# Optimization experiments

Measured on AMD Instinct MI355X. Metric: run time of the kernel, lower is better.

The kernel has to match this reference:

```python
import jax, jax.numpy as jnp
import numpy as np
import math

NUM_HEADS = 16


def setup_inputs() -> dict:
    key = jax.random.key(0)
    ks = jax.random.split(key, 5)
    B, C, H = 2, 2048, 1024
    return {
        "x": jax.random.normal(ks[0], (B, C, H), dtype=jnp.float32),
        "Wqkv_w": jax.random.normal(ks[1], (3 * H, H), dtype=jnp.float32) * (1.0 / math.sqrt(H)),
        "Wqkv_b": jax.random.normal(ks[2], (3 * H,), dtype=jnp.float32) * 0.02,
        "Wo_w": jax.random.normal(ks[3], (H, H), dtype=jnp.float32) * (1.0 / math.sqrt(H)),
        "Wo_b": jax.random.normal(ks[4], (H,), dtype=jnp.float32) * 0.02,
    }


def reference(x, Wqkv_w, Wqkv_b, Wo_w, Wo_b):
    B, C, H = x.shape
    nh = NUM_HEADS
    hd = H // nh
    # QKV projection (torch Linear: x @ W.T + b)
    qkv = x @ Wqkv_w.T + Wqkv_b                      # [B, C, 3H]
    qkv = qkv.reshape(B, C, 3, nh, hd)
    qkv = jnp.transpose(qkv, (2, 0, 3, 1, 4))        # [3, B, nh, C, hd]
    q, k, v = qkv[0], qkv[1], qkv[2]
    scale = 1.0 / math.sqrt(hd)
    att = jnp.einsum('bhqd,bhkd->bhqk', q, k) * scale  # [B, nh, C, C]
    causal = jnp.triu(jnp.ones((C, C), dtype=bool), k=1)  # True above diagonal
    att = jnp.where(causal[None, None], jnp.float32(-jnp.inf), att)
    att = jax.nn.softmax(att, axis=-1)
    # dropout p set to 0 (eval-mode math)
    out = jnp.einsum('bhqk,bhkd->bhqd', att, v)       # [B, nh, C, hd]
    out = jnp.transpose(out, (0, 2, 1, 3)).reshape(B, C, H)
    return out @ Wo_w.T + Wo_b
```

## Files before the change

### kernel.cpp

```cpp
#include <hip/hip_runtime.h>
#include <hip/hip_bf16.h>
#include <math.h>

typedef unsigned short u16;
typedef __attribute__((ext_vector_type(8))) __bf16 bf16x8;
typedef __attribute__((ext_vector_type(4))) float f32x4;
typedef __attribute__((ext_vector_type(8))) unsigned short u16x8;
typedef __attribute__((ext_vector_type(4))) unsigned int u32x4;

__device__ __forceinline__ u16 f2bf(float f) {
  union { float f; unsigned u; } x; x.f = f;
  unsigned r = x.u + 0x7fffu + ((x.u >> 16) & 1u);
  return (u16)(r >> 16);
}

__device__ __forceinline__ void gload16(const u16* g, u16* l) {
  __builtin_amdgcn_global_load_lds(
      (const __attribute__((address_space(1))) void*)g,
      (__attribute__((address_space(3))) void*)l, 16, 0, 0);
}

#define MFMA16(a, b, c) __builtin_amdgcn_mfma_f32_16x16x32_bf16((a), (b), (c), 0, 0, 0)

#define QSCALE 0.18033688011112043f

__global__ __launch_bounds__(256) void cast_all_kernel(
    const float* __restrict__ x, const float* __restrict__ wqkv,
    const float* __restrict__ wo, u16* __restrict__ xb,
    u16* __restrict__ wqb, u16* __restrict__ wob) {
  int i = blockIdx.x * 256 + threadIdx.x;
  const float* src; u16* dst;
  if (i < 1048576)      { src = x;    dst = xb;  }
  else if (i < 1835008) { src = wqkv; dst = wqb; i -= 1048576; }
  else                  { src = wo;   dst = wob; i -= 1835008; }
  f32x4 v = *(const f32x4*)(src + (size_t)i * 4);
  u16 o0 = f2bf(v[0]), o1 = f2bf(v[1]), o2 = f2bf(v[2]), o3 = f2bf(v[3]);
  unsigned lo = (unsigned)o0 | ((unsigned)o1 << 16);
  unsigned hi = (unsigned)o2 | ((unsigned)o3 << 16);
  ((unsigned*)dst)[(size_t)i * 2] = lo;
  ((unsigned*)dst)[(size_t)i * 2 + 1] = hi;
}

__device__ __forceinline__ void gemm_bt_128(
    const u16* __restrict__ A, const u16* __restrict__ B, int K, int m0, int n0,
    u16* As, u16* Bs, f32x4 acc[4][4]) {
  const int tid = threadIdx.x;
  const int lane = tid & 63;
  const int wr = tid >> 7;
  const int wc = (tid >> 6) & 1;
  for (int k0 = 0; k0 < K; k0 += 64) {
    #pragma unroll
    for (int it = 0; it < 4; ++it) {
      int c = it * 256 + tid;
      int row = c >> 3;
      int ko = (c & 7) << 3;
      gload16(A + (size_t)(m0 + row) * K + (k0 + ko), As + c * 8);
      gload16(B + (size_t)(n0 + row) * K + (k0 + ko), Bs + c * 8);
    }
    __syncthreads();
    #pragma unroll
    for (int kk = 0; kk < 2; ++kk) {
      bf16x8 a[4], b[4];
      #pragma unroll
      for (int m = 0; m < 4; ++m)
        a[m] = *(const bf16x8*)(As + ((wr * 64 + m * 16 + (lane & 15)) * 64 +
                                      kk * 32 + ((lane >> 4) << 3)));
      #pragma unroll
      for (int n = 0; n < 4; ++n)
        b[n] = *(const bf16x8*)(Bs + ((wc * 64 + n * 16 + (lane & 15)) * 64 +
                                      kk * 32 + ((lane >> 4) << 3)));
      #pragma unroll
      for (int m = 0; m < 4; ++m)
        #pragma unroll
        for (int n = 0; n < 4; ++n)
          acc[m][n] = MFMA16(a[m], b[n], acc[m][n]);
    }
    __syncthreads();
  }
}

__global__ __launch_bounds__(256) void gemm_qkv_kernel(
    const u16* __restrict__ X, const u16* __restrict__ W, const float* __restrict__ bias,
    u16* __restrict__ Qb, u16* __restrict__ Kb, u16* __restrict__ Vb) {
  __shared__ __align__(16) u16 As[128 * 64];
  __shared__ __align__(16) u16 Bs[128 * 64];
  f32x4 acc[4][4];
  #pragma unroll
  for (int m = 0; m < 4; ++m)
    #pragma unroll
    for (int n = 0; n < 4; ++n) acc[m][n] = (f32x4){0.f, 0.f, 0.f, 0.f};
  const int m0 = blockIdx.y * 128;
  const int n0 = blockIdx.x * 128;
  gemm_bt_128(X, W, 1024, m0, n0, As, Bs, acc);
  const int lane = threadIdx.x & 63;
  const int wr = threadIdx.x >> 7, wc = (threadIdx.x >> 6) & 1;
  #pragma unroll
  for (int m = 0; m < 4; ++m) {
    #pragma unroll
    for (int n = 0; n < 4; ++n) {
      #pragma unroll
      for (int j = 0; j < 4; ++j) {
        int row = m0 + wr * 64 + m * 16 + ((lane >> 4) << 2) + j;
        int col = n0 + wc * 64 + n * 16 + (lane & 15);
        float v = acc[m][n][j] + bias[col];
        int which = col >> 10;
        int rem = col & 1023;
        int h = rem >> 6, d = rem & 63;
        int bb = row >> 11, q = row & 2047;
        if (which == 0) v *= QSCALE;
        u16* dst = (which == 0) ? Qb : (which == 1 ? Kb : Vb);
        dst[((size_t)((bb * 16 + h) * 2048 + q)) * 64 + d] = f2bf(v);
      }
    }
  }
}

__global__ __launch_bounds__(256) void gemm_out_kernel(
    const u16* __restrict__ Ain, const u16* __restrict__ W, const float* __restrict__ bias,
    float* __restrict__ out) {
  __shared__ __align__(16) u16 As[64 * 64];
  __shared__ __align__(16) u16 Bs[128 * 64];
  const int tid = threadIdx.x;
  const int lane = tid & 63;
  const int wc = tid >> 6;
  const int m0 = blockIdx.y * 64;
  const int n0 = blockIdx.x * 128;
  f32x4 acc[4][2] = {};
  for (int k0 = 0; k0 < 1024; k0 += 64) {
    #pragma unroll
    for (int it = 0; it < 2; ++it) {
      int c = it * 256 + tid;
      gload16(Ain + (size_t)(m0 + (c >> 3)) * 1024 + k0 + ((c & 7) << 3), As + c * 8);
    }
    #pragma unroll
    for (int it = 0; it < 4; ++it) {
      int c = it * 256 + tid;
      gload16(W + (size_t)(n0 + (c >> 3)) * 1024 + k0 + ((c & 7) << 3), Bs + c * 8);
    }
    __syncthreads();
    #pragma unroll
    for (int kk = 0; kk < 2; ++kk) {
      bf16x8 a[4], b[2];
      #pragma unroll
      for (int m = 0; m < 4; ++m)
        a[m] = *(const bf16x8*)(As + ((m * 16 + (lane & 15)) * 64 +
                                      kk * 32 + ((lane >> 4) << 3)));
      #pragma unroll
      for (int n = 0; n < 2; ++n)
        b[n] = *(const bf16x8*)(Bs + ((wc * 32 + n * 16 + (lane & 15)) * 64 +
                                      kk * 32 + ((lane >> 4) << 3)));
      #pragma unroll
      for (int m = 0; m < 4; ++m)
        #pragma unroll
        for (int n = 0; n < 2; ++n)
          acc[m][n] = MFMA16(a[m], b[n], acc[m][n]);
    }
    __syncthreads();
  }
  #pragma unroll
  for (int m = 0; m < 4; ++m)
    #pragma unroll
    for (int n = 0; n < 2; ++n)
      #pragma unroll
      for (int j = 0; j < 4; ++j) {
        int row = m0 + m * 16 + ((lane >> 4) << 2) + j;
        int col = n0 + wc * 32 + n * 16 + (lane & 15);
        out[(size_t)row * 1024 + col] = acc[m][n][j] + bias[col];
      }
}

__device__ __forceinline__ void attn_one(
    const u16* __restrict__ Qh, const u16* __restrict__ Kh, const u16* __restrict__ Vh,
    u16* __restrict__ Ob, int bb, int h, int qt,
    u16 (*Ks)[64 * 64], u16 (*Vt)[64 * 64]) {
  const int tid = threadIdx.x, lane = tid & 63, w = tid >> 6;
  const int g = lane >> 4, q15 = lane & 15;

  bf16x8 qf[2];
  const int qrow = qt * 64 + w * 16 + q15;
  #pragma unroll
  for (int kk = 0; kk < 2; ++kk)
    qf[kk] = *(const bf16x8*)(Qh + (size_t)qrow * 64 + kk * 32 + g * 8);

  f32x4 acc_o[4];
  #pragma unroll
  for (int n = 0; n < 4; ++n) acc_o[n] = (f32x4){0.f, 0.f, 0.f, 0.f};
  float m_run = -INFINITY, l_run = 0.f;

  const int nt = qt + 1;

  auto stageK = [&](int t, int buf) {
    #pragma unroll
    for (int it = 0; it < 2; ++it) {
      int c = it * 256 + tid;
      int row = c >> 3, b8 = c & 7;
      gload16(Kh + (size_t)(t * 64 + row) * 64 + ((b8 ^ (row & 7)) << 3),
              Ks[buf] + c * 8);
    }
  };

  stageK(0, 0);
  #pragma unroll
  for (int it = 0; it < 2; ++it) {
    int kloc = it * 32 + (tid >> 3);
    int d0 = (tid & 7) << 3;
    u16x8 v = *(const u16x8*)(Vh + (size_t)kloc * 64 + d0);
    #pragma unroll
    for (int i = 0; i < 8; ++i) {
      int d = d0 + i;
      int fv = (d + (d >> 3)) & 7;
      Vt[0][d * 64 + (((kloc >> 3) ^ fv) << 3) + (kloc & 7)] = v[i];
    }
  }
  __syncthreads();

  for (int t = 0; t < nt; ++t) {
    const int cur = t & 1;
    const bool pre = (t + 1 < nt);
    u16x8 vreg[2];
    if (pre) {
      stageK(t + 1, cur ^ 1);
      #pragma unroll
      for (int it = 0; it < 2; ++it) {
        int kloc = it * 32 + (tid >> 3);
        int d0 = (tid & 7) << 3;
        vreg[it] = *(const u16x8*)(Vh + (size_t)((t + 1) * 64 + kloc) * 64 + d0);
      }
    }

    f32x4 accs[4];
    __builtin_amdgcn_s_setprio(1);
    #pragma unroll
    for (int cb = 0; cb < 4; ++cb) {
      accs[cb] = (f32x4){0.f, 0.f, 0.f, 0.f};
      #pragma unroll
      for (int kk = 0; kk < 2; ++kk) {
        int row = cb * 16 + q15;
        int kblk = kk * 4 + g;
        bf16x8 kf = *(const bf16x8*)(Ks[cur] + row * 64 + ((kblk ^ (row & 7)) << 3));
        accs[cb] = MFMA16(kf, qf[kk], accs[cb]);
      }
    }
    __builtin_amdgcn_s_setprio(0);
    if (t == nt - 1) {
      #pragma unroll
      for (int cb = 0; cb < 4; ++cb)
        #pragma unroll
        for (int j = 0; j < 4; ++j) {
          int kg = t * 64 + cb * 16 + 4 * g + j;
          if (kg > qrow) accs[cb][j] = -INFINITY;
        }
    }

    float mj = accs[0][0];
    #pragma unroll
    for (int cb = 0; cb < 4; ++cb)
      #pragma unroll
      for (int j = 0; j < 4; ++j) mj = fmaxf(mj, accs[cb][j]);
    mj = fmaxf(mj, __shfl_xor(mj, 16));
    mj = fmaxf(mj, __shfl_xor(mj, 32));
    float mn = fmaxf(m_run, mj);
    float sc = exp2f(m_run - mn);
    m_run = mn;
    float rs = 0.f;
    #pragma unroll
    for (int cb = 0; cb < 4; ++cb)
      #pragma unroll
      for (int j = 0; j < 4; ++j) {
        float p = exp2f(accs[cb][j] - mn);
        accs[cb][j] = p;
        rs += p;
      }
    rs += __shfl_xor(rs, 16);
    rs += __shfl_xor(rs, 32);
    l_run = l_run * sc + rs;

    float scj[4];
    #pragma unroll
    for (int j = 0; j < 4; ++j) scj[j] = __shfl(sc, 4 * g + j);
    #pragma unroll
    for (int n = 0; n < 4; ++n)
      #pragma unroll
      for (int j = 0; j < 4; ++j) acc_o[n][j] *= scj[j];

    unsigned Wp[4][2];
    #pragma unroll
    for (int cb = 0; cb < 4; ++cb)
      #pragma unroll
      for (int hh = 0; hh < 2; ++hh)
        asm("v_cvt_pk_bf16_f32 %0, %1, %2"
            : "=v"(Wp[cb][hh]) : "v"(accs[cb][2 * hh]), "v"(accs[cb][2 * hh + 1]));

    unsigned aw[2][4];
    #pragma unroll
    for (int kk = 0; kk < 2; ++kk)
      #pragma unroll
      for (int iw = 0; iw < 4; ++iw) {
        int srcLane = q15 + ((((g & 1) << 1) + (iw >> 1)) << 4);
        unsigned c0 = __shfl(Wp[2 * kk + 0][iw & 1], srcLane);
        unsigned c1 = __shfl(Wp[2 * kk + 1][iw & 1], srcLane);
        aw[kk][iw] = (g >> 1) ? c1 : c0;
      }
    bf16x8 pa0 = __builtin_bit_cast(bf16x8, (u32x4){aw[0][0], aw[0][1], aw[0][2], aw[0][3]});
    bf16x8 pa1 = __builtin_bit_cast(bf16x8, (u32x4){aw[1][0], aw[1][1], aw[1][2], aw[1][3]});

    __builtin_amdgcn_s_setprio(1);
    #pragma unroll
    for (int n = 0; n < 4; ++n) {
      #pragma unroll
      for (int kk = 0; kk < 2; ++kk) {
        int cblk = kk * 4 + g;
        int d = n * 16 + q15;
        int fv = (d + (d >> 3)) & 7;
        bf16x8 vb = *(const bf16x8*)(Vt[cur] + d * 64 + ((cblk ^ fv) << 3));
        acc_o[n] = MFMA16(kk ? pa1 : pa0, vb, acc_o[n]);
      }
    }
    __builtin_amdgcn_s_setprio(0);

    if (pre) {
      #pragma unroll
      for (int it = 0; it < 2; ++it) {
        int kloc = it * 32 + (tid >> 3);
        int d0 = (tid & 7) << 3;
        #pragma unroll
        for (int i = 0; i < 8; ++i) {
          int d = d0 + i;
          int fv = (d + (d >> 3)) & 7;
          Vt[cur ^ 1][d * 64 + (((kloc >> 3) ^ fv) << 3) + (kloc & 7)] = vreg[it][i];
        }
      }
    }
    __syncthreads();
  }

  float invl = 1.0f / l_run;
  float invj[4];
  #pragma unroll
  for (int j = 0; j < 4; ++j) invj[j] = __shfl(invl, 4 * g + j);
  #pragma unroll
  for (int n = 0; n < 4; ++n)
    #pragma unroll
    for (int j = 0; j < 4; ++j) {
      int qg = qt * 64 + w * 16 + 4 * g + j;
      Ob[((size_t)(bb * 2048 + qg)) * 1024 + h * 64 + n * 16 + q15] =
          f2bf(acc_o[n][j] * invj[j]);
    }
}

__global__ __launch_bounds__(256, 4) void attn_kernel(
    const u16* __restrict__ Qb, const u16* __restrict__ Kb, const u16* __restrict__ Vb,
    u16* __restrict__ Ob) {
  __shared__ __align__(16) u16 Ks[2][64 * 64];
  __shared__ __align__(16) u16 Vt[2][64 * 64];
  const int blk = blockIdx.x;
  const int p = blk & 15;
  const int bh = blk >> 4;
  const size_t base = (size_t)bh * 2048 * 64;
  const int bb = bh >> 4, h = bh & 15;
  attn_one(Qb + base, Kb + base, Vb + base, Ob, bb, h, 31 - p, Ks, Vt);
  attn_one(Qb + base, Kb + base, Vb + base, Ob, bb, h, p, Ks, Vt);
}

extern "C" void kernel_launch(void* const* d_in, const int* in_sizes, int n_in,
                              void* d_out, int out_size, void* d_ws, size_t ws_size,
                              hipStream_t stream) {
  const float* x    = (const float*)d_in[0];
  const float* wqkv = (const float*)d_in[1];
  const float* bqkv = (const float*)d_in[2];
  const float* wo   = (const float*)d_in[3];
  const float* bo   = (const float*)d_in[4];
  float* out = (float*)d_out;

  const size_t MB = 1u << 20;
  char* ws = (char*)d_ws;
  u16* x_bf  = (u16*)(ws);
  u16* wq_bf = (u16*)(ws + 8 * MB);
  u16* wo_bf = (u16*)(ws + 14 * MB);
  u16* q_buf = (u16*)(ws + 16 * MB);
  u16* k_buf = (u16*)(ws + 24 * MB);
  u16* v_buf = (u16*)(ws + 32 * MB);
  u16* a_out = (u16*)(ws + 40 * MB);

  cast_all_kernel<<<8192, 256, 0, stream>>>(x, wqkv, wo, x_bf, wq_bf, wo_bf);

  gemm_qkv_kernel<<<dim3(24, 32), 256, 0, stream>>>(x_bf, wq_bf, bqkv,
                                                    q_buf, k_buf, v_buf);
  attn_kernel<<<512, 256, 0, stream>>>(q_buf, k_buf, v_buf, a_out);
  gemm_out_kernel<<<dim3(8, 64), 256, 0, stream>>>(a_out, wo_bf, bo, out);
}
```

Baseline: 151.4 us.

## Store V transposed in QKV GEMM and load K/V fragments directly from global

The QKV projection epilogue now writes V in a transposed [head, d, seq] layout. The attention kernel then drops its LDS staging of K and V and instead loads MFMA fragments straight from global memory into registers, prefetching the next K tile. This removes the LDS transpose scatter and the __syncthreads barriers. In exchange, each wave redundantly reads whole K/V tiles from global/L2, register use rises, the occupancy hint drops to 2, and the transposed V store is uncoalesced.

Result: slower. 215.2 us (+42.1%).

```diff
diff --git a/kernel.cpp b/kernel.cpp
--- a/kernel.cpp
+++ b/kernel.cpp
@@ -81,7 +81,7 @@
 
 __global__ __launch_bounds__(256) void gemm_qkv_kernel(
     const u16* __restrict__ X, const u16* __restrict__ W, const float* __restrict__ bias,
-    u16* __restrict__ Qb, u16* __restrict__ Kb, u16* __restrict__ Vb) {
+    u16* __restrict__ Qb, u16* __restrict__ Kb, u16* __restrict__ VTb) {
   __shared__ __align__(16) u16 As[128 * 64];
   __shared__ __align__(16) u16 Bs[128 * 64];
   f32x4 acc[4][4];
@@ -107,9 +107,14 @@
         int rem = col & 1023;
         int h = rem >> 6, d = rem & 63;
         int bb = row >> 11, q = row & 2047;
-        if (which == 0) v *= QSCALE;
-        u16* dst = (which == 0) ? Qb : (which == 1 ? Kb : Vb);
-        dst[((size_t)((bb * 16 + h) * 2048 + q)) * 64 + d] = f2bf(v);
+        int hh = bb * 16 + h;
+        if (which == 0) {
+          Qb[((size_t)hh * 2048 + q) * 64 + d] = f2bf(v * QSCALE);
+        } else if (which == 1) {
+          Kb[((size_t)hh * 2048 + q) * 64 + d] = f2bf(v);
+        } else {
+          VTb[((size_t)hh * 64 + d) * 2048 + q] = f2bf(v);
+        }
       }
     }
   }
@@ -170,14 +175,13 @@
 }
 
 __device__ __forceinline__ void attn_one(
-    const u16* __restrict__ Qh, const u16* __restrict__ Kh, const u16* __restrict__ Vh,
-    u16* __restrict__ Ob, int bb, int h, int qt,
-    u16 (*Ks)[64 * 64], u16 (*Vt)[64 * 64]) {
+    const u16* __restrict__ Qh, const u16* __restrict__ Kh, const u16* __restrict__ VTh,
+    u16* __restrict__ Ob, int bb, int h, int qt) {
   const int tid = threadIdx.x, lane = tid & 63, w = tid >> 6;
   const int g = lane >> 4, q15 = lane & 15;
+  const int qrow = qt * 64 + w * 16 + q15;
 
   bf16x8 qf[2];
-  const int qrow = qt * 64 + w * 16 + q15;
   #pragma unroll
   for (int kk = 0; kk < 2; ++kk)
     qf[kk] = *(const bf16x8*)(Qh + (size_t)qrow * 64 + kk * 32 + g * 8);
@@ -189,44 +193,30 @@
 
   const int nt = qt + 1;
 
-  auto stageK = [&](int t, int buf) {
-    #pragma unroll
-    for (int it = 0; it < 2; ++it) {
-      int c = it * 256 + tid;
-      int row = c >> 3, b8 = c & 7;
-      gload16(Kh + (size_t)(t * 64 + row) * 64 + ((b8 ^ (row & 7)) << 3),
-              Ks[buf] + c * 8);
-    }
-  };
-
-  stageK(0, 0);
-  #pragma unroll
-  for (int it = 0; it < 2; ++it) {
-    int kloc = it * 32 + (tid >> 3);
-    int d0 = (tid & 7) << 3;
-    u16x8 v = *(const u16x8*)(Vh + (size_t)kloc * 64 + d0);
-    #pragma unroll
-    for (int i = 0; i < 8; ++i) {
-      int d = d0 + i;
-      int fv = (d + (d >> 3)) & 7;
-      Vt[0][d * 64 + (((kloc >> 3) ^ fv) << 3) + (kloc & 7)] = v[i];
-    }
-  }
-  __syncthreads();
+  bf16x8 kc[4][2];
+  #pragma unroll
+  for (int cb = 0; cb < 4; ++cb)
+    #pragma unroll
+    for (int kk = 0; kk < 2; ++kk)
+      kc[cb][kk] = *(const bf16x8*)(Kh + (size_t)(cb * 16 + q15) * 64 + kk * 32 + g * 8);
 
   for (int t = 0; t < nt; ++t) {
-    const int cur = t & 1;
-    const bool pre = (t + 1 < nt);
-    u16x8 vreg[2];
-    if (pre) {
-      stageK(t + 1, cur ^ 1);
-      #pragma unroll
-      for (int it = 0; it < 2; ++it) {
-        int kloc = it * 32 + (tid >> 3);
-        int d0 = (tid & 7) << 3;
-        vreg[it] = *(const u16x8*)(Vh + (size_t)((t + 1) * 64 + kloc) * 64 + d0);
-      }
-    }
+    bf16x8 kn[4][2];
+    if (t + 1 < nt) {
+      #pragma unroll
+      for (int cb = 0; cb < 4; ++cb)
+        #pragma unroll
+        for (int kk = 0; kk < 2; ++kk)
+          kn[cb][kk] = *(const bf16x8*)(Kh +
+              (size_t)((t + 1) * 64 + cb * 16 + q15) * 64 + kk * 32 + g * 8);
+    }
+    bf16x8 vf[4][2];
+    #pragma unroll
+    for (int n = 0; n < 4; ++n)
+      #pragma unroll
+      for (int kk = 0; kk < 2; ++kk)
+        vf[n][kk] = *(const bf16x8*)(VTh +
+            (size_t)(n * 16 + q15) * 2048 + t * 64 + kk * 32 + g * 8);
 
     f32x4 accs[4];
     __builtin_amdgcn_s_setprio(1);
@@ -234,14 +224,11 @@
     for (int cb = 0; cb < 4; ++cb) {
       accs[cb] = (f32x4){0.f, 0.f, 0.f, 0.f};
       #pragma unroll
-      for (int kk = 0; kk < 2; ++kk) {
-        int row = cb * 16 + q15;
-        int kblk = kk * 4 + g;
-        bf16x8 kf = *(const bf16x8*)(Ks[cur] + row * 64 + ((kblk ^ (row & 7)) << 3));
-        accs[cb] = MFMA16(kf, qf[kk], accs[cb]);
-      }
+      for (int kk = 0; kk < 2; ++kk)
+        accs[cb] = MFMA16(kc[cb][kk], qf[kk], accs[cb]);
     }
     __builtin_amdgcn_s_setprio(0);
+
     if (t == nt - 1) {
       #pragma unroll
       for (int cb = 0; cb < 4; ++cb)
@@ -307,31 +294,18 @@
     __builtin_amdgcn_s_setprio(1);
     #pragma unroll
     for (int n = 0; n < 4; ++n) {
-      #pragma unroll
-      for (int kk = 0; kk < 2; ++kk) {
-        int cblk = kk * 4 + g;
-        int d = n * 16 + q15;
-        int fv = (d + (d >> 3)) & 7;
-        bf16x8 vb = *(const bf16x8*)(Vt[cur] + d * 64 + ((cblk ^ fv) << 3));
-        acc_o[n] = MFMA16(kk ? pa1 : pa0, vb, acc_o[n]);
-      }
+      acc_o[n] = MFMA16(pa0, vf[n][0], acc_o[n]);
+      acc_o[n] = MFMA16(pa1, vf[n][1], acc_o[n]);
     }
     __builtin_amdgcn_s_setprio(0);
 
-    if (pre) {
-      #pragma unroll
-      for (int it = 0; it < 2; ++it) {
-        int kloc = it * 32 + (tid >> 3);
-        int d0 = (tid & 7) << 3;
-        #pragma unroll
-        for (int i = 0; i < 8; ++i) {
-          int d = d0 + i;
-          int fv = (d + (d >> 3)) & 7;
-          Vt[cur ^ 1][d * 64 + (((kloc >> 3) ^ fv) << 3) + (kloc & 7)] = vreg[it][i];
-        }
-      }
-    }
-    __syncthreads();
+    if (t + 1 < nt) {
+      #pragma unroll
+      for (int cb = 0; cb < 4; ++cb)
+        #pragma unroll
+        for (int kk = 0; kk < 2; ++kk)
+          kc[cb][kk] = kn[cb][kk];
+    }
   }
 
   float invl = 1.0f / l_run;
@@ -348,18 +322,16 @@
     }
 }
 
-__global__ __launch_bounds__(256, 4) void attn_kernel(
-    const u16* __restrict__ Qb, const u16* __restrict__ Kb, const u16* __restrict__ Vb,
+__global__ __launch_bounds__(256, 2) void attn_kernel(
+    const u16* __restrict__ Qb, const u16* __restrict__ Kb, const u16* __restrict__ VTb,
     u16* __restrict__ Ob) {
-  __shared__ __align__(16) u16 Ks[2][64 * 64];
-  __shared__ __align__(16) u16 Vt[2][64 * 64];
   const int blk = blockIdx.x;
   const int p = blk & 15;
   const int bh = blk >> 4;
   const size_t base = (size_t)bh * 2048 * 64;
   const int bb = bh >> 4, h = bh & 15;
-  attn_one(Qb + base, Kb + base, Vb + base, Ob, bb, h, 31 - p, Ks, Vt);
-  attn_one(Qb + base, Kb + base, Vb + base, Ob, bb, h, p, Ks, Vt);
+  attn_one(Qb + base, Kb + base, VTb + base, Ob, bb, h, 31 - p);
+  attn_one(Qb + base, Kb + base, VTb + base, Ob, bb, h, p);
 }
 
 extern "C" void kernel_launch(void* const* d_in, const int* in_sizes, int n_in,
@@ -379,13 +351,13 @@
   u16* wo_bf = (u16*)(ws + 14 * MB);
   u16* q_buf = (u16*)(ws + 16 * MB);
   u16* k_buf = (u16*)(ws + 24 * MB);
-  u16* v_buf = (u16*)(ws + 32 * MB);
+  u16* vt_buf= (u16*)(ws + 32 * MB);
   u16* a_out = (u16*)(ws + 40 * MB);
 
   cast_all_kernel<<<8192, 256, 0, stream>>>(x, wqkv, wo, x_bf, wq_bf, wo_bf);
 
   gemm_qkv_kernel<<<dim3(24, 32), 256, 0, stream>>>(x_bf, wq_bf, bqkv,
-                                                    q_buf, k_buf, v_buf);
-  attn_kernel<<<512, 256, 0, stream>>>(q_buf, k_buf, v_buf, a_out);
+                                                    q_buf, k_buf, vt_buf);
+  attn_kernel<<<512, 256, 0, stream>>>(q_buf, k_buf, vt_buf, a_out);
   gemm_out_kernel<<<dim3(8, 64), 256, 0, stream>>>(a_out, wo_bf, bo, out);
 }
```

## Triple-buffer K/V tiles in attention with two-tile-ahead prefetch

Applied to the files above, without the earlier changes.

Deepens the attention kernel's K/V software pipeline from double to triple buffering. K tiles and V registers are now prefetched two iterations ahead, and buffer indices rotate each step. The per-iteration __syncthreads is replaced by inline s_waitcnt with a partial vmcnt plus s_barrier, so later loads can stay in flight across the barrier. The cost is 1.5x more LDS per block (48KB), which may cap resident blocks per CU below the launch-bounds target. The hand-counted vmcnt value also depends on the exact number of memory instructions the compiler emits.

After: 151.2 us. About the same (-0.2%).

```diff
diff --git a/kernel.cpp b/kernel.cpp
--- a/kernel.cpp
+++ b/kernel.cpp
@@ -198,35 +198,45 @@
               Ks[buf] + c * 8);
     }
   };
-
-  stageK(0, 0);
-  #pragma unroll
-  for (int it = 0; it < 2; ++it) {
-    int kloc = it * 32 + (tid >> 3);
-    int d0 = (tid & 7) << 3;
-    u16x8 v = *(const u16x8*)(Vh + (size_t)kloc * 64 + d0);
-    #pragma unroll
-    for (int i = 0; i < 8; ++i) {
-      int d = d0 + i;
-      int fv = (d + (d >> 3)) & 7;
-      Vt[0][d * 64 + (((kloc >> 3) ^ fv) << 3) + (kloc & 7)] = v[i];
-    }
-  }
-  __syncthreads();
-
+  auto loadV = [&](int t, u16x8 vreg[2]) {
+    #pragma unroll
+    for (int it = 0; it < 2; ++it) {
+      int kloc = it * 32 + (tid >> 3);
+      int d0 = (tid & 7) << 3;
+      vreg[it] = *(const u16x8*)(Vh + (size_t)(t * 64 + kloc) * 64 + d0);
+    }
+  };
+  auto writeV = [&](const u16x8 vreg[2], int buf) {
+    #pragma unroll
+    for (int it = 0; it < 2; ++it) {
+      int kloc = it * 32 + (tid >> 3);
+      int d0 = (tid & 7) << 3;
+      #pragma unroll
+      for (int i = 0; i < 8; ++i) {
+        int d = d0 + i;
+        int fv = (d + (d >> 3)) & 7;
+        Vt[buf][d * 64 + (((kloc >> 3) ^ fv) << 3) + (kloc & 7)] = vreg[it][i];
+      }
+    }
+  };
+
+  u16x8 vcur[2];
+  {
+    stageK(0, 0);
+    u16x8 v0[2];
+    loadV(0, v0);
+    if (nt > 1) { stageK(1, 1); loadV(1, vcur); }
+    writeV(v0, 0);
+    if (nt > 1) asm volatile("s_waitcnt vmcnt(6) lgkmcnt(0)\ns_barrier" ::: "memory");
+    else        asm volatile("s_waitcnt vmcnt(0) lgkmcnt(0)\ns_barrier" ::: "memory");
+  }
+
+  int b0 = 0, b1 = 1, b2 = 2;
   for (int t = 0; t < nt; ++t) {
-    const int cur = t & 1;
-    const bool pre = (t + 1 < nt);
-    u16x8 vreg[2];
-    if (pre) {
-      stageK(t + 1, cur ^ 1);
-      #pragma unroll
-      for (int it = 0; it < 2; ++it) {
-        int kloc = it * 32 + (tid >> 3);
-        int d0 = (tid & 7) << 3;
-        vreg[it] = *(const u16x8*)(Vh + (size_t)((t + 1) * 64 + kloc) * 64 + d0);
-      }
-    }
+    const bool pre2 = (t + 2 < nt);
+    const bool pre1 = (t + 1 < nt);
+    u16x8 vnext[2];
+    if (pre2) { stageK(t + 2, b2); loadV(t + 2, vnext); }
 
     f32x4 accs[4];
     __builtin_amdgcn_s_setprio(1);
@@ -237,7 +247,7 @@
       for (int kk = 0; kk < 2; ++kk) {
         int row = cb * 16 + q15;
         int kblk = kk * 4 + g;
-        bf16x8 kf = *(const bf16x8*)(Ks[cur] + row * 64 + ((kblk ^ (row & 7)) << 3));
+        bf16x8 kf = *(const bf16x8*)(Ks[b0] + row * 64 + ((kblk ^ (row & 7)) << 3));
         accs[cb] = MFMA16(kf, qf[kk], accs[cb]);
       }
     }
@@ -312,26 +322,21 @@
         int cblk = kk * 4 + g;
         int d = n * 16 + q15;
         int fv = (d + (d >> 3)) & 7;
-        bf16x8 vb = *(const bf16x8*)(Vt[cur] + d * 64 + ((cblk ^ fv) << 3));
+        bf16x8 vb = *(const bf16x8*)(Vt[b0] + d * 64 + ((cblk ^ fv) << 3));
         acc_o[n] = MFMA16(kk ? pa1 : pa0, vb, acc_o[n]);
       }
     }
     __builtin_amdgcn_s_setprio(0);
 
-    if (pre) {
-      #pragma unroll
-      for (int it = 0; it < 2; ++it) {
-        int kloc = it * 32 + (tid >> 3);
-        int d0 = (tid & 7) << 3;
-        #pragma unroll
-        for (int i = 0; i < 8; ++i) {
-          int d = d0 + i;
-          int fv = (d + (d >> 3)) & 7;
-          Vt[cur ^ 1][d * 64 + (((kloc >> 3) ^ fv) << 3) + (kloc & 7)] = vreg[it][i];
-        }
-      }
-    }
-    __syncthreads();
+    if (pre1) {
+      writeV(vcur, b1);
+      if (pre2) { vcur[0] = vnext[0]; vcur[1] = vnext[1]; }
+    }
+
+    if (pre2) asm volatile("s_waitcnt vmcnt(6) lgkmcnt(0)\ns_barrier" ::: "memory");
+    else      asm volatile("s_waitcnt vmcnt(0) lgkmcnt(0)\ns_barrier" ::: "memory");
+
+    int tmp = b0; b0 = b1; b1 = b2; b2 = tmp;
   }
 
   float invl = 1.0f / l_run;
@@ -351,8 +356,8 @@
 __global__ __launch_bounds__(256, 4) void attn_kernel(
     const u16* __restrict__ Qb, const u16* __restrict__ Kb, const u16* __restrict__ Vb,
     u16* __restrict__ Ob) {
-  __shared__ __align__(16) u16 Ks[2][64 * 64];
-  __shared__ __align__(16) u16 Vt[2][64 * 64];
+  __shared__ __align__(16) u16 Ks[3][64 * 64];
+  __shared__ __align__(16) u16 Vt[3][64 * 64];
   const int blk = blockIdx.x;
   const int p = blk & 15;
   const int bh = blk >> 4;
```

## Stage QKV epilogue through LDS for vectorized stores; add lazy softmax rescale

Applied to the files above, without the earlier changes.

The QKV GEMM epilogue now writes its bias-added, scaled bf16 results into a padded shared-memory tile and then stores them as 16-byte vectors per row, instead of issuing scattered 2-byte global stores. This targets the store traffic of the head-split layout. The attention kernel also skips the running-max update and the output rescale when every lane's new block max exceeds the running max by no more than 8 (in log2 units), which cuts exp and multiply work. The cost is a bounded growth of unnormalized values before normalization, plus an extra barrier and reuse of shared memory in the GEMM epilogue.

New measurement: 147.7 us. 1.03x faster.

```diff
diff --git a/kernel.cpp b/kernel.cpp
--- a/kernel.cpp
+++ b/kernel.cpp
@@ -82,8 +82,7 @@
 __global__ __launch_bounds__(256) void gemm_qkv_kernel(
     const u16* __restrict__ X, const u16* __restrict__ W, const float* __restrict__ bias,
     u16* __restrict__ Qb, u16* __restrict__ Kb, u16* __restrict__ Vb) {
-  __shared__ __align__(16) u16 As[128 * 64];
-  __shared__ __align__(16) u16 Bs[128 * 64];
+  __shared__ __align__(16) u16 S[17408];
   f32x4 acc[4][4];
   #pragma unroll
   for (int m = 0; m < 4; ++m)
@@ -91,27 +90,38 @@
     for (int n = 0; n < 4; ++n) acc[m][n] = (f32x4){0.f, 0.f, 0.f, 0.f};
   const int m0 = blockIdx.y * 128;
   const int n0 = blockIdx.x * 128;
-  gemm_bt_128(X, W, 1024, m0, n0, As, Bs, acc);
-  const int lane = threadIdx.x & 63;
-  const int wr = threadIdx.x >> 7, wc = (threadIdx.x >> 6) & 1;
-  #pragma unroll
-  for (int m = 0; m < 4; ++m) {
-    #pragma unroll
-    for (int n = 0; n < 4; ++n) {
+  gemm_bt_128(X, W, 1024, m0, n0, S, S + 8192, acc);
+
+  const int tid = threadIdx.x;
+  const int lane = tid & 63;
+  const int wr = tid >> 7, wc = (tid >> 6) & 1;
+  const int which = n0 >> 10;
+  const float qs = (which == 0) ? QSCALE : 1.0f;
+  u16* __restrict__ dst = (which == 0) ? Qb : (which == 1 ? Kb : Vb);
+
+  #pragma unroll
+  for (int m = 0; m < 4; ++m)
+    #pragma unroll
+    for (int n = 0; n < 4; ++n)
       #pragma unroll
       for (int j = 0; j < 4; ++j) {
-        int row = m0 + wr * 64 + m * 16 + ((lane >> 4) << 2) + j;
-        int col = n0 + wc * 64 + n * 16 + (lane & 15);
-        float v = acc[m][n][j] + bias[col];
-        int which = col >> 10;
-        int rem = col & 1023;
-        int h = rem >> 6, d = rem & 63;
-        int bb = row >> 11, q = row & 2047;
-        if (which == 0) v *= QSCALE;
-        u16* dst = (which == 0) ? Qb : (which == 1 ? Kb : Vb);
-        dst[((size_t)((bb * 16 + h) * 2048 + q)) * 64 + d] = f2bf(v);
-      }
-    }
+        int row = wr * 64 + m * 16 + ((lane >> 4) << 2) + j;
+        int col = wc * 64 + n * 16 + (lane & 15);
+        float v = (acc[m][n][j] + bias[n0 + col]) * qs;
+        S[row * 136 + col] = f2bf(v);
+      }
+  __syncthreads();
+
+  #pragma unroll
+  for (int i = 0; i < 8; ++i) {
+    int c = i * 256 + tid;
+    int row = c >> 4, ch = c & 15;
+    u16x8 val = *(const u16x8*)(S + row * 136 + ch * 8);
+    int grow = m0 + row;
+    int bb = grow >> 11, q = grow & 2047;
+    int gcol = n0 + ch * 8;
+    int h = (gcol >> 6) & 15, d0 = gcol & 63;
+    *(u16x8*)(dst + ((size_t)((bb * 16 + h) * 2048 + q)) * 64 + d0) = val;
   }
 }
 
@@ -259,29 +269,31 @@
       for (int j = 0; j < 4; ++j) mj = fmaxf(mj, accs[cb][j]);
     mj = fmaxf(mj, __shfl_xor(mj, 16));
     mj = fmaxf(mj, __shfl_xor(mj, 32));
-    float mn = fmaxf(m_run, mj);
-    float sc = exp2f(m_run - mn);
-    m_run = mn;
+    if (!__all(mj - m_run <= 8.0f)) {
+      float mn = fmaxf(m_run, mj);
+      float sc = exp2f(m_run - mn);
+      m_run = mn;
+      l_run *= sc;
+      float scj[4];
+      #pragma unroll
+      for (int j = 0; j < 4; ++j) scj[j] = __shfl(sc, 4 * g + j);
+      #pragma unroll
+      for (int n = 0; n < 4; ++n)
+        #pragma unroll
+        for (int j = 0; j < 4; ++j) acc_o[n][j] *= scj[j];
+    }
     float rs = 0.f;
     #pragma unroll
     for (int cb = 0; cb < 4; ++cb)
       #pragma unroll
       for (int j = 0; j < 4; ++j) {
-        float p = exp2f(accs[cb][j] - mn);
+        float p = exp2f(accs[cb][j] - m_run);
         accs[cb][j] = p;
         rs += p;
       }
     rs += __shfl_xor(rs, 16);
     rs += __shfl_xor(rs, 32);
-    l_run = l_run * sc + rs;
-
-    float scj[4];
-    #pragma unroll
-    for (int j = 0; j < 4; ++j) scj[j] = __shfl(sc, 4 * g + j);
-    #pragma unroll
-    for (int n = 0; n < 4; ++n)
-      #pragma unroll
-      for (int j = 0; j < 4; ++j) acc_o[n][j] *= scj[j];
+    l_run += rs;
 
     unsigned Wp[4][2];
     #pragma unroll
```
